# Performance work log

Measured on AMD Instinct MI355X. Metric: run time of the kernel, lower is better.

The kernel has to match this reference:

```python
import jax, jax.numpy as jnp
import numpy as np

N_NODES = 100000
N_EDGES = 800000
D_FEAT = 64
OBS_FRAC = 0.3  # fraction of observed (nonzero) entries in x


def setup_inputs() -> dict:
    key = jax.random.key(0)
    k1, k2, k3, k4 = jax.random.split(key, 4)
    # sparse-valued feature matrix: zeros = missing entries to be imputed
    x = jax.random.uniform(k1, (N_NODES, D_FEAT), dtype=jnp.float32)
    observed = jax.random.uniform(k2, (N_NODES, D_FEAT)) < OBS_FRAC
    x = jnp.where(observed, x, 0.0)
    # COO sparse adjacency: row (destination of aggregation), col (source)
    row = jax.random.randint(k3, (N_EDGES,), 0, N_NODES)
    col = jax.random.randint(k4, (N_EDGES,), 0, N_NODES)
    edge_index = jnp.stack([row, col]).astype(jnp.int64)
    # row-normalized weights (row-stochastic adjacency, stable diffusion)
    deg = jax.ops.segment_sum(jnp.ones((N_EDGES,), jnp.float32), row,
                              num_segments=N_NODES)
    edge_weight = 1.0 / jnp.maximum(deg, 1.0)[row]
    return {
        "x": x,
        "edge_weight": edge_weight,
        "edge_index": edge_index,
        "iter_steps": 10,
        "mask": 1,
    }


def reference(x, edge_weight, edge_index, iter_steps, mask):
    # x: [N, D]; edge_index: [2, E] (row, col) of sparse_adj; edge_weight: [E]
    N = x.shape[0]
    row, col = edge_index[0], edge_index[1]
    known = x != 0  # torch.nonzero(original_x) positions

    out = x
    for _ in range(iter_steps):
        # out_new[i] = sum_{e: row[e]==i} w[e] * out[col[e]]  == sparse.mm(adj, out)
        msg = edge_weight[:, None] * out[col]          # [E, D]
        out = jax.ops.segment_sum(msg, row, num_segments=N)
        if mask:
            # reset observed entries to their original values
            out = jnp.where(known, x, out)
    return out
```

## Files before the change

### kernel.cpp

```cpp
#include <hip/hip_runtime.h>
#include <hip/hip_bf16.h>
#include <hip/hip_fp16.h>


namespace {

constexpr int N = 100000;
constexpr int E = 800000;
constexpr int D = 64;

constexpr int SCAN_BLK = 1024;
constexpr int NSCAN = (N + SCAN_BLK - 1) / SCAN_BLK;

__global__ void hist_k(const int* __restrict__ row, int* __restrict__ deg) {
  int e = blockIdx.x * blockDim.x + threadIdx.x;
  if (e < E) atomicAdd(&deg[row[e]], 1);
}

__global__ void scan1_k(const int* __restrict__ deg, int* __restrict__ row_ptr,
                        int* __restrict__ blockSums) {
  __shared__ int sh[SCAN_BLK];
  int tid = threadIdx.x;
  int i = blockIdx.x * SCAN_BLK + tid;
  sh[tid] = (i < N) ? deg[i] : 0;
  __syncthreads();
  for (int off = 1; off < SCAN_BLK; off <<= 1) {
    int t = (tid >= off) ? sh[tid - off] : 0;
    __syncthreads();
    sh[tid] += t;
    __syncthreads();
  }
  if (i < N) row_ptr[i + 1] = sh[tid];
  if (tid == SCAN_BLK - 1) blockSums[blockIdx.x] = sh[tid];
}

__global__ void scan2_k(int* __restrict__ blockSums) {
  if (threadIdx.x == 0 && blockIdx.x == 0) {
    int acc = 0;
    for (int b = 0; b < NSCAN; ++b) {
      int t = blockSums[b];
      blockSums[b] = acc;
      acc += t;
    }
  }
}

__global__ void scan3_k(int* __restrict__ row_ptr, const int* __restrict__ blockSums,
                        int* __restrict__ pos) {
  int i = blockIdx.x * blockDim.x + threadIdx.x;
  if (i == 0) row_ptr[0] = 0;
  if (i < N) {
    int v = row_ptr[i + 1] + blockSums[i / SCAN_BLK];
    row_ptr[i + 1] = v;
  }
}

__global__ void posinit_k(const int* __restrict__ row_ptr, int* __restrict__ pos) {
  int i = blockIdx.x * blockDim.x + threadIdx.x;
  if (i < N) pos[i] = row_ptr[i];
}

__global__ void scatter_k(const int* __restrict__ row, const int* __restrict__ col,
                          const float* __restrict__ w, int* __restrict__ pos,
                          int2* __restrict__ ed) {
  int e = blockIdx.x * blockDim.x + threadIdx.x;
  if (e < E) {
    int r = row[e];
    int p = atomicAdd(&pos[r], 1);
    int2 pk;
    pk.x = col[e];
    pk.y = __float_as_int(w[e]);
    ed[p] = pk;
  }
}

template <typename SrcT, typename DstT>
__global__ void prop_k(const SrcT* __restrict__ src, DstT* __restrict__ dst,
                       const float* __restrict__ x,
                       const int* __restrict__ row_ptr,
                       const int2* __restrict__ ed) {
  int wave = threadIdx.x >> 6;
  int lane = threadIdx.x & 63;
  int i = blockIdx.x * (blockDim.x >> 6) + wave;
  if (i >= N) return;
  int s = row_ptr[i];
  int t = row_ptr[i + 1];
  float acc = 0.f;
  int e = s;
  for (; e + 4 <= t; e += 4) {
    int2 p0 = ed[e + 0];
    int2 p1 = ed[e + 1];
    int2 p2 = ed[e + 2];
    int2 p3 = ed[e + 3];
    float v0 = (float)src[(size_t)p0.x * D + lane];
    float v1 = (float)src[(size_t)p1.x * D + lane];
    float v2 = (float)src[(size_t)p2.x * D + lane];
    float v3 = (float)src[(size_t)p3.x * D + lane];
    acc += __int_as_float(p0.y) * v0;
    acc += __int_as_float(p1.y) * v1;
    acc += __int_as_float(p2.y) * v2;
    acc += __int_as_float(p3.y) * v3;
  }
  for (; e < t; ++e) {
    int2 p0 = ed[e];
    acc += __int_as_float(p0.y) * (float)src[(size_t)p0.x * D + lane];
  }
  float xv = x[(size_t)i * D + lane];
  float o = (xv != 0.f) ? xv : acc;
  dst[(size_t)i * D + lane] = (DstT)o;
}

}

extern "C" void kernel_launch(void* const* d_in, const int* in_sizes, int n_in,
                              void* d_out, int out_size, void* d_ws, size_t ws_size,
                              hipStream_t stream) {
  const float* x = (const float*)d_in[0];
  const float* w = (const float*)d_in[1];
  const int* ei = (const int*)d_in[2];
  const int* row = ei;
  const int* col = ei + E;

  char* ws = (char*)d_ws;
  size_t off = 0;
  auto alloc = [&](size_t bytes) -> void* {
    void* p = ws + off;
    off = (off + bytes + 255) & ~(size_t)255;
    return p;
  };
  __half* h0   = (__half*)alloc((size_t)N * D * sizeof(__half));
  __half* h1   = (__half*)alloc((size_t)N * D * sizeof(__half));
  int* deg     = (int*)alloc((size_t)N * sizeof(int));
  int* row_ptr = (int*)alloc((size_t)(N + 1) * sizeof(int));
  int* pos     = (int*)alloc((size_t)N * sizeof(int));
  int* bsums   = (int*)alloc((size_t)NSCAN * sizeof(int));
  int2* ed     = (int2*)alloc((size_t)E * sizeof(int2));

  hipMemsetAsync(deg, 0, (size_t)N * sizeof(int), stream);
  hist_k<<<(E + 255) / 256, 256, 0, stream>>>(row, deg);
  scan1_k<<<NSCAN, SCAN_BLK, 0, stream>>>(deg, row_ptr, bsums);
  scan2_k<<<1, 64, 0, stream>>>(bsums);
  scan3_k<<<(N + 255) / 256, 256, 0, stream>>>(row_ptr, bsums, pos);
  posinit_k<<<(N + 255) / 256, 256, 0, stream>>>(row_ptr, pos);
  scatter_k<<<(E + 255) / 256, 256, 0, stream>>>(row, col, w, pos, ed);

  constexpr int BLOCKS = (N + 3) / 4;
  float* out = (float*)d_out;
  prop_k<float, __half><<<BLOCKS, 256, 0, stream>>>(x, h0, x, row_ptr, ed);
  __half* cur = h0;
  __half* alt = h1;
  for (int it = 1; it < 9; ++it) {
    prop_k<__half, __half><<<BLOCKS, 256, 0, stream>>>(cur, alt, x, row_ptr, ed);
    __half* tmp = cur; cur = alt; alt = tmp;
  }
  prop_k<__half, float><<<BLOCKS, 256, 0, stream>>>(cur, out, x, row_ptr, ed);
}
```

Before: 567.0 us.

## Precompute known-entry bitmask and skip writes to observed entries

Adds an init kernel that copies x into both fp16 ping-pong buffers and the fp32 output, and stores one 64-bit ballot mask per node marking observed entries. Each propagation step then reads that mask instead of the full fp32 x row and writes only the unobserved entries, so observed values stay fixed from init. The gather loop is also unrolled to 8 edges to keep more loads in flight. The trade-off is one extra init pass, a first iteration that reads x through fp16 rather than fp32, and masked partial stores.

Result: faster. 518.2 us (-8.6%).

```diff
diff --git a/kernel.cpp b/kernel.cpp
--- a/kernel.cpp
+++ b/kernel.cpp
@@ -1,6 +1,7 @@
 #include <hip/hip_runtime.h>
 #include <hip/hip_bf16.h>
 #include <hip/hip_fp16.h>
+#include <stdint.h>
 
 
 namespace {
@@ -45,14 +46,10 @@
   }
 }
 
-__global__ void scan3_k(int* __restrict__ row_ptr, const int* __restrict__ blockSums,
-                        int* __restrict__ pos) {
+__global__ void scan3_k(int* __restrict__ row_ptr, const int* __restrict__ blockSums) {
   int i = blockIdx.x * blockDim.x + threadIdx.x;
   if (i == 0) row_ptr[0] = 0;
-  if (i < N) {
-    int v = row_ptr[i + 1] + blockSums[i / SCAN_BLK];
-    row_ptr[i + 1] = v;
-  }
+  if (i < N) row_ptr[i + 1] += blockSums[i / SCAN_BLK];
 }
 
 __global__ void posinit_k(const int* __restrict__ row_ptr, int* __restrict__ pos) {
@@ -74,40 +71,68 @@
   }
 }
 
-template <typename SrcT, typename DstT>
-__global__ void prop_k(const SrcT* __restrict__ src, DstT* __restrict__ dst,
-                       const float* __restrict__ x,
+__global__ void init_k(const float* __restrict__ x, __half* __restrict__ h0,
+                       __half* __restrict__ h1, float* __restrict__ out,
+                       uint64_t* __restrict__ kmask) {
+  int wave = threadIdx.x >> 6;
+  int lane = threadIdx.x & 63;
+  int i = blockIdx.x * (blockDim.x >> 6) + wave;
+  if (i >= N) return;
+  size_t idx = (size_t)i * D + lane;
+  float xv = x[idx];
+  __half hv = __float2half(xv);
+  h0[idx] = hv;
+  h1[idx] = hv;
+  out[idx] = xv;
+  uint64_t m = __ballot(xv != 0.f);
+  if (lane == 0) kmask[i] = m;
+}
+
+template <typename DstT>
+__global__ void prop_k(const __half* __restrict__ src, DstT* __restrict__ dst,
+                       const uint64_t* __restrict__ kmask,
                        const int* __restrict__ row_ptr,
                        const int2* __restrict__ ed) {
   int wave = threadIdx.x >> 6;
   int lane = threadIdx.x & 63;
   int i = blockIdx.x * (blockDim.x >> 6) + wave;
   if (i >= N) return;
+  uint64_t m = kmask[i];
   int s = row_ptr[i];
   int t = row_ptr[i + 1];
   float acc = 0.f;
   int e = s;
+  for (; e + 8 <= t; e += 8) {
+    int2 p0 = ed[e + 0]; int2 p1 = ed[e + 1]; int2 p2 = ed[e + 2]; int2 p3 = ed[e + 3];
+    int2 p4 = ed[e + 4]; int2 p5 = ed[e + 5]; int2 p6 = ed[e + 6]; int2 p7 = ed[e + 7];
+    float v0 = __half2float(src[(size_t)p0.x * D + lane]);
+    float v1 = __half2float(src[(size_t)p1.x * D + lane]);
+    float v2 = __half2float(src[(size_t)p2.x * D + lane]);
+    float v3 = __half2float(src[(size_t)p3.x * D + lane]);
+    float v4 = __half2float(src[(size_t)p4.x * D + lane]);
+    float v5 = __half2float(src[(size_t)p5.x * D + lane]);
+    float v6 = __half2float(src[(size_t)p6.x * D + lane]);
+    float v7 = __half2float(src[(size_t)p7.x * D + lane]);
+    acc += __int_as_float(p0.y) * v0; acc += __int_as_float(p1.y) * v1;
+    acc += __int_as_float(p2.y) * v2; acc += __int_as_float(p3.y) * v3;
+    acc += __int_as_float(p4.y) * v4; acc += __int_as_float(p5.y) * v5;
+    acc += __int_as_float(p6.y) * v6; acc += __int_as_float(p7.y) * v7;
+  }
   for (; e + 4 <= t; e += 4) {
-    int2 p0 = ed[e + 0];
-    int2 p1 = ed[e + 1];
-    int2 p2 = ed[e + 2];
-    int2 p3 = ed[e + 3];
-    float v0 = (float)src[(size_t)p0.x * D + lane];
-    float v1 = (float)src[(size_t)p1.x * D + lane];
-    float v2 = (float)src[(size_t)p2.x * D + lane];
-    float v3 = (float)src[(size_t)p3.x * D + lane];
-    acc += __int_as_float(p0.y) * v0;
-    acc += __int_as_float(p1.y) * v1;
-    acc += __int_as_float(p2.y) * v2;
-    acc += __int_as_float(p3.y) * v3;
+    int2 p0 = ed[e + 0]; int2 p1 = ed[e + 1]; int2 p2 = ed[e + 2]; int2 p3 = ed[e + 3];
+    float v0 = __half2float(src[(size_t)p0.x * D + lane]);
+    float v1 = __half2float(src[(size_t)p1.x * D + lane]);
+    float v2 = __half2float(src[(size_t)p2.x * D + lane]);
+    float v3 = __half2float(src[(size_t)p3.x * D + lane]);
+    acc += __int_as_float(p0.y) * v0; acc += __int_as_float(p1.y) * v1;
+    acc += __int_as_float(p2.y) * v2; acc += __int_as_float(p3.y) * v3;
   }
   for (; e < t; ++e) {
     int2 p0 = ed[e];
-    acc += __int_as_float(p0.y) * (float)src[(size_t)p0.x * D + lane];
+    acc += __int_as_float(p0.y) * __half2float(src[(size_t)p0.x * D + lane]);
   }
-  float xv = x[(size_t)i * D + lane];
-  float o = (xv != 0.f) ? xv : acc;
-  dst[(size_t)i * D + lane] = (DstT)o;
+  if (!((m >> lane) & 1ull))
+    dst[(size_t)i * D + lane] = (DstT)acc;
 }
 
 }
@@ -128,30 +153,32 @@
     off = (off + bytes + 255) & ~(size_t)255;
     return p;
   };
-  __half* h0   = (__half*)alloc((size_t)N * D * sizeof(__half));
-  __half* h1   = (__half*)alloc((size_t)N * D * sizeof(__half));
-  int* deg     = (int*)alloc((size_t)N * sizeof(int));
-  int* row_ptr = (int*)alloc((size_t)(N + 1) * sizeof(int));
-  int* pos     = (int*)alloc((size_t)N * sizeof(int));
-  int* bsums   = (int*)alloc((size_t)NSCAN * sizeof(int));
-  int2* ed     = (int2*)alloc((size_t)E * sizeof(int2));
+  __half* h0     = (__half*)alloc((size_t)N * D * sizeof(__half));
+  __half* h1     = (__half*)alloc((size_t)N * D * sizeof(__half));
+  uint64_t* kmsk = (uint64_t*)alloc((size_t)N * sizeof(uint64_t));
+  int* deg       = (int*)alloc((size_t)N * sizeof(int));
+  int* row_ptr   = (int*)alloc((size_t)(N + 1) * sizeof(int));
+  int* pos       = (int*)alloc((size_t)N * sizeof(int));
+  int* bsums     = (int*)alloc((size_t)NSCAN * sizeof(int));
+  int2* ed       = (int2*)alloc((size_t)E * sizeof(int2));
+
+  constexpr int BLOCKS = (N + 3) / 4;
+  float* out = (float*)d_out;
 
   hipMemsetAsync(deg, 0, (size_t)N * sizeof(int), stream);
   hist_k<<<(E + 255) / 256, 256, 0, stream>>>(row, deg);
   scan1_k<<<NSCAN, SCAN_BLK, 0, stream>>>(deg, row_ptr, bsums);
   scan2_k<<<1, 64, 0, stream>>>(bsums);
-  scan3_k<<<(N + 255) / 256, 256, 0, stream>>>(row_ptr, bsums, pos);
+  scan3_k<<<(N + 255) / 256, 256, 0, stream>>>(row_ptr, bsums);
   posinit_k<<<(N + 255) / 256, 256, 0, stream>>>(row_ptr, pos);
   scatter_k<<<(E + 255) / 256, 256, 0, stream>>>(row, col, w, pos, ed);
+  init_k<<<BLOCKS, 256, 0, stream>>>(x, h0, h1, out, kmsk);
 
-  constexpr int BLOCKS = (N + 3) / 4;
-  float* out = (float*)d_out;
-  prop_k<float, __half><<<BLOCKS, 256, 0, stream>>>(x, h0, x, row_ptr, ed);
   __half* cur = h0;
   __half* alt = h1;
-  for (int it = 1; it < 9; ++it) {
-    prop_k<__half, __half><<<BLOCKS, 256, 0, stream>>>(cur, alt, x, row_ptr, ed);
+  for (int it = 0; it < 9; ++it) {
+    prop_k<__half><<<BLOCKS, 256, 0, stream>>>(cur, alt, kmsk, row_ptr, ed);
     __half* tmp = cur; cur = alt; alt = tmp;
   }
-  prop_k<__half, float><<<BLOCKS, 256, 0, stream>>>(cur, out, x, row_ptr, ed);
+  prop_k<float><<<BLOCKS, 256, 0, stream>>>(cur, out, kmsk, row_ptr, ed);
 }
```
